# Optimization experiments

Hardware: AMD Instinct MI355X
Metric: run time of the kernel (lower is better)

## Reference

```python
import jax, jax.numpy as jnp
import numpy as np

N_EMB = 512
EMB_DIM = 64
DECAY = 0.99
EPS = 1e-5


def setup_inputs() -> dict:
    key = jax.random.key(0)
    k1, k2 = jax.random.split(key)
    x = jax.random.normal(k1, (32, EMB_DIM, 64, 64), dtype=jnp.float32)
    weight = jax.random.uniform(k2, (EMB_DIM, N_EMB), dtype=jnp.float32)  # rd_init=True: torch.rand(emb_dim, n_emb)
    cluster_size = jnp.zeros((N_EMB,), dtype=jnp.float32)
    embed_avg = weight  # buffer initialized as embed.clone()
    return {"x": x, "weight": weight, "cluster_size": cluster_size, "embed_avg": embed_avg}


def reference(x, weight, cluster_size, embed_avg):
    B, D, H, W = x.shape
    n_emb = weight.shape[1]
    # (B, D, H, W) -> (N, D) tokens
    flat = jnp.transpose(x, (0, 2, 3, 1)).reshape(-1, D)
    dist = (jnp.sum(flat * flat, axis=1, keepdims=True)
            - 2.0 * (flat @ weight)
            + jnp.sum(weight * weight, axis=0)[None, :])
    argmin = jnp.argmin(dist, axis=1)                      # (N,)
    quant = jnp.take(weight.T, argmin, axis=0)             # gather -> (N, D)
    result = jnp.transpose(quant.reshape(B, H, W, D), (0, 3, 1, 2))  # (B, D, H, W)

    # --- EMA codebook update (training branch) ---
    ones = jnp.ones(argmin.shape, dtype=x.dtype)
    n_idx = jax.ops.segment_sum(ones, argmin, num_segments=n_emb)    # onehot.sum(0)
    n_idx = jnp.where(n_idx == 0, jnp.ones_like(n_idx), n_idx)       # clamp empty clusters to 1
    new_cluster_size = DECAY * cluster_size + (1.0 - DECAY) * n_idx
    embed_sum = jax.ops.segment_sum(flat, argmin, num_segments=n_emb).T  # flatten.T @ onehot -> (D, n_emb)
    new_embed_avg = DECAY * embed_avg + (1.0 - DECAY) * embed_sum
    n = jnp.sum(new_cluster_size)
    cs = (new_cluster_size + EPS) / (n + n_emb * EPS) * n
    new_weight = new_embed_avg / cs[None, :]

    return result, argmin.reshape(B, H, W), new_weight, new_cluster_size, new_embed_avg
```

## Files before the change

kernel.cpp:

```cpp
#include <hip/hip_runtime.h>

#define NEMB 512
#define EMB 64
#define BSTR 262144
#define DECAYF 0.99f
#define OMDF 0.01f
#define EPSF 1e-5f
#define GAP_T 0.012f
#define QCAP 32768

typedef __attribute__((ext_vector_type(8))) short bf16x8;
typedef __attribute__((ext_vector_type(4))) float f32x4;

__device__ __forceinline__ unsigned short f2bf(float f) {
    unsigned u = __float_as_uint(f);
    return (unsigned short)((u + 0x7FFFu + ((u >> 16) & 1u)) >> 16);
}
__device__ __forceinline__ float bf2f(unsigned short h) {
    return __uint_as_float(((unsigned)h) << 16);
}

__global__ void prep_kernel(const float* __restrict__ w,
                            unsigned short* __restrict__ wh, unsigned short* __restrict__ wl,
                            float* __restrict__ wsq,
                            float* __restrict__ cnt_ws, float* __restrict__ es_region,
                            unsigned* __restrict__ gcnt) {
    int j = threadIdx.x;
    if (blockIdx.x < 8) {
        int d0 = blockIdx.x << 3;
        bf16x8 hb, lb;
#pragma unroll
        for (int i = 0; i < 8; ++i) {
            float v = w[(d0 + i) * NEMB + j];
            unsigned short h = f2bf(v);
            hb[i] = (short)h;
            lb[i] = (short)f2bf(v - bf2f(h));
        }
        *(bf16x8*)(wh + j * EMB + d0) = hb;
        *(bf16x8*)(wl + j * EMB + d0) = lb;
    } else {
        float s = 0.f;
#pragma unroll
        for (int d = 0; d < EMB; ++d) { float v = w[d * NEMB + j]; s = fmaf(v, v, s); }
        wsq[j] = s;
        cnt_ws[j] = 0.f;
        if (j == 0) *gcnt = 0u;
#pragma unroll
        for (int k = j; k < 32768; k += 512) es_region[k] = 0.f;
    }
}

#define UPD(S1, J1, S2, J2, s_, j_) do { \
    if (s_ < S1 || (s_ == S1 && j_ < J1)) { S2 = S1; J2 = J1; S1 = s_; J1 = j_; } \
    else if (s_ < S2 || (s_ == S2 && j_ < J2)) { S2 = s_; J2 = j_; } } while (0)

__global__ __launch_bounds__(128, 4) void vq_main(
    const float* __restrict__ x,
    const unsigned short* __restrict__ wh, const unsigned short* __restrict__ wl,
    const float* __restrict__ wsq,
    float* __restrict__ out_arg, unsigned* __restrict__ gcnt, int* __restrict__ queue)
{
    __shared__ float wsq_s[NEMB];

    const int tid = threadIdx.x;
    const int blk = blockIdx.x;
    const int b   = blk >> 6;
    const int h   = blk & 63;
    const int t0  = b * 4096 + h * 64;
    const float* xrow = x + b * BSTR + h * 64;

    wsq_s[tid]       = wsq[tid];
    wsq_s[tid + 128] = wsq[tid + 128];
    wsq_s[tid + 256] = wsq[tid + 256];
    wsq_s[tid + 384] = wsq[tid + 384];

    const int lane = tid & 63;
    const int wave = tid >> 6;
    const int l15  = lane & 15;
    const int quad = lane >> 4;
    const int wbase = wave << 5;

    bf16x8 ah[2][2], al[2][2];
    float  xq[2][4];
#pragma unroll
    for (int mt = 0; mt < 2; ++mt) {
        const float* xp = xrow + wbase + (mt << 4) + l15;
        float s = 0.f;
#pragma unroll
        for (int ks = 0; ks < 2; ++ks) {
            const int d0 = (ks << 5) + (quad << 3);
            bf16x8 hh, ll;
#pragma unroll
            for (int i = 0; i < 8; ++i) {
                float v = xp[(d0 + i) * 4096];
                s = fmaf(v, v, s);
                unsigned short hb = f2bf(v);
                hh[i] = (short)hb;
                ll[i] = (short)f2bf(v - bf2f(hb));
            }
            ah[mt][ks] = hh; al[mt][ks] = ll;
        }
        s += __shfl_xor(s, 16, 64);
        s += __shfl_xor(s, 32, 64);
#pragma unroll
        for (int r = 0; r < 4; ++r)
            xq[mt][r] = __shfl(s, (quad << 2) + r, 64);
    }
    __syncthreads();

    float v1[2][4], v2[2][4];
    int   j1[2][4];
#pragma unroll
    for (int mt = 0; mt < 2; ++mt)
#pragma unroll
        for (int r = 0; r < 4; ++r) { v1[mt][r] = 3.4e38f; v2[mt][r] = 3.4e38f; j1[mt][r] = 0; }

    const unsigned short* ph = wh + l15 * EMB + (quad << 3);
    const unsigned short* pl = wl + l15 * EMB + (quad << 3);
    bf16x8 nb0 = *(const bf16x8*)(ph);
    bf16x8 nb1 = *(const bf16x8*)(ph + 32);
    bf16x8 nb2 = *(const bf16x8*)(pl);
    bf16x8 nb3 = *(const bf16x8*)(pl + 32);

#pragma unroll 2
    for (int it = 0; it < 32; ++it) {
        bf16x8 b0 = nb0, b1 = nb1, b2 = nb2, b3 = nb3;
        if (it != 31) {
            ph += 1024; pl += 1024;
            nb0 = *(const bf16x8*)(ph);
            nb1 = *(const bf16x8*)(ph + 32);
            nb2 = *(const bf16x8*)(pl);
            nb3 = *(const bf16x8*)(pl + 32);
        }
        const int n = (it << 4) + l15;
        float wq = wsq_s[n];

        f32x4 acc0 = (f32x4){0.f, 0.f, 0.f, 0.f};
        f32x4 acc1 = (f32x4){0.f, 0.f, 0.f, 0.f};
        acc0 = __builtin_amdgcn_mfma_f32_16x16x32_bf16(ah[0][0], b0, acc0, 0, 0, 0);
        acc1 = __builtin_amdgcn_mfma_f32_16x16x32_bf16(ah[1][0], b0, acc1, 0, 0, 0);
        acc0 = __builtin_amdgcn_mfma_f32_16x16x32_bf16(ah[0][1], b1, acc0, 0, 0, 0);
        acc1 = __builtin_amdgcn_mfma_f32_16x16x32_bf16(ah[1][1], b1, acc1, 0, 0, 0);
        acc0 = __builtin_amdgcn_mfma_f32_16x16x32_bf16(ah[0][0], b2, acc0, 0, 0, 0);
        acc1 = __builtin_amdgcn_mfma_f32_16x16x32_bf16(ah[1][0], b2, acc1, 0, 0, 0);
        acc0 = __builtin_amdgcn_mfma_f32_16x16x32_bf16(ah[0][1], b3, acc0, 0, 0, 0);
        acc1 = __builtin_amdgcn_mfma_f32_16x16x32_bf16(ah[1][1], b3, acc1, 0, 0, 0);
        acc0 = __builtin_amdgcn_mfma_f32_16x16x32_bf16(al[0][0], b0, acc0, 0, 0, 0);
        acc1 = __builtin_amdgcn_mfma_f32_16x16x32_bf16(al[1][0], b0, acc1, 0, 0, 0);
        acc0 = __builtin_amdgcn_mfma_f32_16x16x32_bf16(al[0][1], b1, acc0, 0, 0, 0);
        acc1 = __builtin_amdgcn_mfma_f32_16x16x32_bf16(al[1][1], b1, acc1, 0, 0, 0);

#pragma unroll
        for (int r = 0; r < 4; ++r) {
            float s0 = fmaf(-2.f, acc0[r], xq[0][r] + wq);
            bool p0 = s0 < v1[0][r];
            float mx0 = fmaxf(s0, v1[0][r]);
            v1[0][r] = fminf(s0, v1[0][r]);
            v2[0][r] = fminf(v2[0][r], mx0);
            j1[0][r] = p0 ? n : j1[0][r];

            float s1 = fmaf(-2.f, acc1[r], xq[1][r] + wq);
            bool p1 = s1 < v1[1][r];
            float mx1 = fmaxf(s1, v1[1][r]);
            v1[1][r] = fminf(s1, v1[1][r]);
            v2[1][r] = fminf(v2[1][r], mx1);
            j1[1][r] = p1 ? n : j1[1][r];
        }
    }

#pragma unroll
    for (int mt = 0; mt < 2; ++mt)
#pragma unroll
        for (int r = 0; r < 4; ++r) {
            float a1 = v1[mt][r], a2 = v2[mt][r];
            int   aj = j1[mt][r];
#pragma unroll
            for (int msk = 1; msk < 16; msk <<= 1) {
                float o1 = __shfl_xor(a1, msk, 64);
                int   oj = __shfl_xor(aj, msk, 64);
                float o2 = __shfl_xor(a2, msk, 64);
                bool take = (o1 < a1) || (o1 == a1 && oj < aj);
                float mx = fmaxf(a1, o1);
                a2 = fminf(fminf(a2, o2), mx);
                a1 = fminf(a1, o1);
                aj = take ? oj : aj;
            }
            v1[mt][r] = a1; v2[mt][r] = a2; j1[mt][r] = aj;
        }

    if (l15 == 0) {
#pragma unroll
        for (int mt = 0; mt < 2; ++mt)
#pragma unroll
            for (int r = 0; r < 4; ++r) {
                int gt = t0 + wbase + (mt << 4) + (quad << 2) + r;
                out_arg[gt] = (float)j1[mt][r];
                if (v2[mt][r] - v1[mt][r] < GAP_T) {
                    unsigned idx = atomicAdd(gcnt, 1u);
                    if (idx < QCAP) queue[idx] = gt;
                }
            }
    }
}

__global__ __launch_bounds__(256) void refine_kernel(
    const float* __restrict__ x, const float* __restrict__ w,
    const float* __restrict__ wsq, const unsigned* __restrict__ gcnt,
    const int* __restrict__ queue, float* __restrict__ out_arg)
{
    __shared__ float wsq_s[NEMB];
    const int tid = threadIdx.x;
    wsq_s[tid] = wsq[tid];
    wsq_s[tid + 256] = wsq[tid + 256];
    __syncthreads();

    unsigned nfu = *gcnt;
    const int nf = (int)(nfu < (unsigned)QCAP ? nfu : (unsigned)QCAP);
    const int lane = tid & 63;
    const int gw = (blockIdx.x << 2) + (tid >> 6);

    for (int i = gw; i < nf; i += 1024) {
        const int t = queue[i];
        const int b = t >> 12, pos = t & 4095;
        float xd = x[b * BSTR + lane * 4096 + pos];
        float xqv = xd * xd;
#pragma unroll
        for (int mk = 1; mk < 64; mk <<= 1) xqv += __shfl_xor(xqv, mk, 64);

        float accv[8];
#pragma unroll
        for (int k = 0; k < 8; ++k) accv[k] = 0.f;
#pragma unroll 4
        for (int d = 0; d < EMB; ++d) {
            float4 wa = *(const float4*)(w + d * NEMB + (lane << 2));
            float4 wb = *(const float4*)(w + d * NEMB + 256 + (lane << 2));
            float xv = __shfl(xd, d, 64);
            accv[0] = fmaf(xv, wa.x, accv[0]);
            accv[1] = fmaf(xv, wa.y, accv[1]);
            accv[2] = fmaf(xv, wa.z, accv[2]);
            accv[3] = fmaf(xv, wa.w, accv[3]);
            accv[4] = fmaf(xv, wb.x, accv[4]);
            accv[5] = fmaf(xv, wb.y, accv[5]);
            accv[6] = fmaf(xv, wb.z, accv[6]);
            accv[7] = fmaf(xv, wb.w, accv[7]);
        }

        float S1 = 3.4e38f, S2 = 3.4e38f; int J1 = 0, J2 = 0;
#pragma unroll
        for (int k = 0; k < 8; ++k) {
            int j = (k < 4) ? ((lane << 2) + k) : (256 + (lane << 2) + k - 4);
            float s = (xqv - 2.f * accv[k]) + wsq_s[j];
            UPD(S1, J1, S2, J2, s, j);
        }
#pragma unroll
        for (int mk = 1; mk < 64; mk <<= 1) {
            float os1 = __shfl_xor(S1, mk, 64); int oj1 = __shfl_xor(J1, mk, 64);
            float os2 = __shfl_xor(S2, mk, 64); int oj2 = __shfl_xor(J2, mk, 64);
            UPD(S1, J1, S2, J2, os1, oj1);
            UPD(S1, J1, S2, J2, os2, oj2);
        }

        int jm = J1;
        if (S2 - S1 < 1e-3f) {
            float w1 = w[lane * NEMB + J1];
            float w2 = w[lane * NEMB + J2];
            double e1 = (double)w1 * (double)w1 - 2.0 * (double)xd * (double)w1;
            double e2 = (double)w2 * (double)w2 - 2.0 * (double)xd * (double)w2;
#pragma unroll
            for (int mk = 1; mk < 64; mk <<= 1) {
                e1 += __shfl_xor(e1, mk, 64);
                e2 += __shfl_xor(e2, mk, 64);
            }
            if (e2 < e1 || (e2 == e1 && J2 < J1)) jm = J2;
        }
        if (lane == 0) out_arg[t] = (float)jm;
    }
}

__global__ __launch_bounds__(256) void finish_kernel(
    const float* __restrict__ x, const float* __restrict__ w, const float* __restrict__ arg,
    float* __restrict__ out_result,
    float* __restrict__ es, float* __restrict__ cnt)
{
    __shared__ float wrow[NEMB];
    __shared__ float acc[8][513];
    const int tid = threadIdx.x;
    const int grp = blockIdx.x >> 5;
    const int chunk = blockIdx.x & 31;

    float* af = &acc[0][0];
#pragma unroll
    for (int k = tid; k < 8 * 513; k += 256) af[k] = 0.f;
    if (grp < 64) {
        wrow[tid] = w[grp * NEMB + tid];
        wrow[tid + 256] = w[grp * NEMB + tid + 256];
    }
    __syncthreads();

    const int c = tid & 7;
    const int tbase = chunk << 12;
    if (grp < 64) {
        const int d = grp;
#pragma unroll 2
        for (int it = 0; it < 4; ++it) {
            int t = tbase + (it << 10) + (tid << 2);
            int o = (t >> 12) * BSTR + d * 4096 + (t & 4095);
            float4 a4 = *(const float4*)(arg + t);
            float4 x4 = *(const float4*)(x + o);
            int j0 = (int)a4.x, j1 = (int)a4.y, j2 = (int)a4.z, j3 = (int)a4.w;
            atomicAdd(&acc[c][j0], x4.x);
            atomicAdd(&acc[c][j1], x4.y);
            atomicAdd(&acc[c][j2], x4.z);
            atomicAdd(&acc[c][j3], x4.w);
            float4 r4 = {wrow[j0], wrow[j1], wrow[j2], wrow[j3]};
            *(float4*)(out_result + o) = r4;
        }
    } else {
#pragma unroll 2
        for (int it = 0; it < 4; ++it) {
            int t = tbase + (it << 10) + (tid << 2);
            float4 a4 = *(const float4*)(arg + t);
            atomicAdd(&acc[c][(int)a4.x], 1.0f);
            atomicAdd(&acc[c][(int)a4.y], 1.0f);
            atomicAdd(&acc[c][(int)a4.z], 1.0f);
            atomicAdd(&acc[c][(int)a4.w], 1.0f);
        }
    }
    __syncthreads();

    float* dst = (grp < 64) ? (es + grp * NEMB) : cnt;
#pragma unroll
    for (int k = 0; k < 2; ++k) {
        int j = tid + (k << 8);
        float v = acc[0][j] + acc[1][j] + acc[2][j] + acc[3][j]
                + acc[4][j] + acc[5][j] + acc[6][j] + acc[7][j];
        if (v != 0.f) atomicAdd(&dst[j], v);
    }
}

__global__ void finalize_kernel(const float* __restrict__ cs_in, const float* __restrict__ avg_in,
                                const float* __restrict__ cnt_ws,
                                float* __restrict__ out_w, float* __restrict__ out_ncs,
                                float* __restrict__ avg_io ) {
    __shared__ float red[NEMB];
    const int j = threadIdx.x;
    const int d = blockIdx.x;
    float c = cnt_ws[j];
    float nidx = (c == 0.f) ? 1.f : c;
    float ncs = DECAYF * cs_in[j] + OMDF * nidx;
    red[j] = ncs;
    __syncthreads();
    for (int s = 256; s > 0; s >>= 1) {
        if (j < s) red[j] += red[j + s];
        __syncthreads();
    }
    float n = red[0];
    float csj = (ncs + EPSF) / (n + (float)NEMB * EPSF) * n;
    int o = d * NEMB + j;
    float esv = avg_io[o];
    float navg = DECAYF * avg_in[o] + OMDF * esv;
    avg_io[o] = navg;
    out_w[o] = navg / csj;
    if (d == 0) out_ncs[j] = ncs;
}

extern "C" void kernel_launch(void* const* d_in, const int* in_sizes, int n_in,
                              void* d_out, int out_size, void* d_ws, size_t ws_size,
                              hipStream_t stream) {
    (void)in_sizes; (void)n_in; (void)out_size; (void)ws_size;
    const float* x   = (const float*)d_in[0];
    const float* w   = (const float*)d_in[1];
    const float* cs  = (const float*)d_in[2];
    const float* avg = (const float*)d_in[3];

    float* out = (float*)d_out;
    float* out_result = out;
    float* out_arg    = out + 8388608;
    float* out_w      = out + 8519680;
    float* out_ncs    = out + 8552448;
    float* out_avg    = out + 8552960;

    char* wsb = (char*)d_ws;
    unsigned short* wh = (unsigned short*)wsb;
    unsigned short* wl = (unsigned short*)(wsb + 65536);
    float* wsq      = (float*)(wsb + 131072);
    float* cnt_ws   = (float*)(wsb + 133120);
    unsigned* gcnt  = (unsigned*)(wsb + 135168);
    int* queue      = (int*)(wsb + 135232);

    prep_kernel<<<9, 512, 0, stream>>>(w, wh, wl, wsq, cnt_ws, out_avg, gcnt);
    vq_main<<<2048, 128, 0, stream>>>(x, wh, wl, wsq, out_arg, gcnt, queue);
    refine_kernel<<<256, 256, 0, stream>>>(x, w, wsq, gcnt, queue, out_arg);
    finish_kernel<<<2080, 256, 0, stream>>>(x, w, out_arg, out_result, out_avg, cnt_ws);
    finalize_kernel<<<64, 512, 0, stream>>>(cs, avg, cnt_ws, out_w, out_ncs, out_avg);
}
```

Before: 214.3 us.

## Stage x and codebook tiles in LDS, enlarge vq and finish blocks

Measured after the change: 189.7 us. -11.5%, faster.

```diff
diff --git a/kernel.cpp b/kernel.cpp
--- a/kernel.cpp
+++ b/kernel.cpp
@@ -54,25 +54,42 @@
     if (s_ < S1 || (s_ == S1 && j_ < J1)) { S2 = S1; J2 = J1; S1 = s_; J1 = j_; } \
     else if (s_ < S2 || (s_ == S2 && j_ < J2)) { S2 = s_; J2 = j_; } } while (0)
 
-__global__ __launch_bounds__(128, 4) void vq_main(
+__global__ __launch_bounds__(512, 4) void vq_main(
     const float* __restrict__ x,
     const unsigned short* __restrict__ wh, const unsigned short* __restrict__ wl,
     const float* __restrict__ wsq,
     float* __restrict__ out_arg, unsigned* __restrict__ gcnt, int* __restrict__ queue)
 {
+    __shared__ __align__(16) unsigned char ubuf[65536];
     __shared__ float wsq_s[NEMB];
+    __shared__ float xsq_s[256];
+
+    float* xt = (float*)ubuf;
+    unsigned short* whs = (unsigned short*)ubuf;
+    unsigned short* wls = whs + 16384;
 
     const int tid = threadIdx.x;
     const int blk = blockIdx.x;
-    const int b   = blk >> 6;
-    const int h   = blk & 63;
-    const int t0  = b * 4096 + h * 64;
-    const float* xrow = x + b * BSTR + h * 64;
-
-    wsq_s[tid]       = wsq[tid];
-    wsq_s[tid + 128] = wsq[tid + 128];
-    wsq_s[tid + 256] = wsq[tid + 256];
-    wsq_s[tid + 384] = wsq[tid + 384];
+    const int b    = blk >> 4;
+    const int hgrp = blk & 15;
+    const int t0 = b * 4096 + hgrp * 256;
+    const float* xbase = x + b * BSTR + hgrp * 256;
+
+#pragma unroll
+    for (int it = 0; it < 8; ++it) {
+        int idx = tid + (it << 9);
+        int d = idx >> 6, q = idx & 63;
+        *(float4*)(xt + d * 256 + (q << 2)) = *(const float4*)(xbase + d * 4096 + (q << 2));
+    }
+    wsq_s[tid] = wsq[tid];
+    __syncthreads();
+
+    if (tid < 256) {
+        float s = 0.f;
+#pragma unroll
+        for (int d = 0; d < EMB; ++d) { float v = xt[d * 256 + tid]; s = fmaf(v, v, s); }
+        xsq_s[tid] = s;
+    }
 
     const int lane = tid & 63;
     const int wave = tid >> 6;
@@ -81,32 +98,31 @@
     const int wbase = wave << 5;
 
     bf16x8 ah[2][2], al[2][2];
-    float  xq[2][4];
 #pragma unroll
     for (int mt = 0; mt < 2; ++mt) {
-        const float* xp = xrow + wbase + (mt << 4) + l15;
-        float s = 0.f;
+        int m = wbase + (mt << 4) + l15;
 #pragma unroll
         for (int ks = 0; ks < 2; ++ks) {
-            const int d0 = (ks << 5) + (quad << 3);
+            int k0 = (ks << 5) + (quad << 3);
             bf16x8 hh, ll;
 #pragma unroll
             for (int i = 0; i < 8; ++i) {
-                float v = xp[(d0 + i) * 4096];
-                s = fmaf(v, v, s);
-                unsigned short hb = f2bf(v);
-                hh[i] = (short)hb;
-                ll[i] = (short)f2bf(v - bf2f(hb));
+                float v = xt[(k0 + i) * 256 + m];
+                unsigned short h = f2bf(v);
+                hh[i] = (short)h;
+                ll[i] = (short)f2bf(v - bf2f(h));
             }
             ah[mt][ks] = hh; al[mt][ks] = ll;
         }
-        s += __shfl_xor(s, 16, 64);
-        s += __shfl_xor(s, 32, 64);
+    }
+    __syncthreads();
+
+    float xq[2][4];
+#pragma unroll
+    for (int mt = 0; mt < 2; ++mt)
 #pragma unroll
         for (int r = 0; r < 4; ++r)
-            xq[mt][r] = __shfl(s, (quad << 2) + r, 64);
-    }
-    __syncthreads();
+            xq[mt][r] = xsq_s[wbase + (mt << 4) + (quad << 2) + r];
 
     float v1[2][4], v2[2][4];
     int   j1[2][4];
@@ -115,57 +131,70 @@
 #pragma unroll
         for (int r = 0; r < 4; ++r) { v1[mt][r] = 3.4e38f; v2[mt][r] = 3.4e38f; j1[mt][r] = 0; }
 
-    const unsigned short* ph = wh + l15 * EMB + (quad << 3);
-    const unsigned short* pl = wl + l15 * EMB + (quad << 3);
-    bf16x8 nb0 = *(const bf16x8*)(ph);
-    bf16x8 nb1 = *(const bf16x8*)(ph + 32);
-    bf16x8 nb2 = *(const bf16x8*)(pl);
-    bf16x8 nb3 = *(const bf16x8*)(pl + 32);
-
+    const int m7 = l15 & 7;
+    const int s0off = ((quad ^ m7) << 3);
+    const int s1off = (((4 | quad) ^ m7) << 3);
+
+    for (int half = 0; half < 2; ++half) {
+#pragma unroll
+        for (int it = 0; it < 8; ++it) {
+            int e = tid + (it << 9);
+            int arr  = e >> 11;
+            int win  = e & 2047;
+            int row  = win >> 3;
+            int slot = win & 7;
+            const unsigned short* src =
+                (arr ? wl : wh) + ((half << 8) + row) * EMB + (slot << 3);
+            bf16x8 v = *(const bf16x8*)src;
+            unsigned short* dstb = arr ? wls : whs;
+            *(bf16x8*)(dstb + row * EMB + ((slot ^ (row & 7)) << 3)) = v;
+        }
+        __syncthreads();
+
+        const int nbase = half << 8;
 #pragma unroll 2
-    for (int it = 0; it < 32; ++it) {
-        bf16x8 b0 = nb0, b1 = nb1, b2 = nb2, b3 = nb3;
-        if (it != 31) {
-            ph += 1024; pl += 1024;
-            nb0 = *(const bf16x8*)(ph);
-            nb1 = *(const bf16x8*)(ph + 32);
-            nb2 = *(const bf16x8*)(pl);
-            nb3 = *(const bf16x8*)(pl + 32);
-        }
-        const int n = (it << 4) + l15;
-        float wq = wsq_s[n];
-
-        f32x4 acc0 = (f32x4){0.f, 0.f, 0.f, 0.f};
-        f32x4 acc1 = (f32x4){0.f, 0.f, 0.f, 0.f};
-        acc0 = __builtin_amdgcn_mfma_f32_16x16x32_bf16(ah[0][0], b0, acc0, 0, 0, 0);
-        acc1 = __builtin_amdgcn_mfma_f32_16x16x32_bf16(ah[1][0], b0, acc1, 0, 0, 0);
-        acc0 = __builtin_amdgcn_mfma_f32_16x16x32_bf16(ah[0][1], b1, acc0, 0, 0, 0);
-        acc1 = __builtin_amdgcn_mfma_f32_16x16x32_bf16(ah[1][1], b1, acc1, 0, 0, 0);
-        acc0 = __builtin_amdgcn_mfma_f32_16x16x32_bf16(ah[0][0], b2, acc0, 0, 0, 0);
-        acc1 = __builtin_amdgcn_mfma_f32_16x16x32_bf16(ah[1][0], b2, acc1, 0, 0, 0);
-        acc0 = __builtin_amdgcn_mfma_f32_16x16x32_bf16(ah[0][1], b3, acc0, 0, 0, 0);
-        acc1 = __builtin_amdgcn_mfma_f32_16x16x32_bf16(ah[1][1], b3, acc1, 0, 0, 0);
-        acc0 = __builtin_amdgcn_mfma_f32_16x16x32_bf16(al[0][0], b0, acc0, 0, 0, 0);
-        acc1 = __builtin_amdgcn_mfma_f32_16x16x32_bf16(al[1][0], b0, acc1, 0, 0, 0);
-        acc0 = __builtin_amdgcn_mfma_f32_16x16x32_bf16(al[0][1], b1, acc0, 0, 0, 0);
-        acc1 = __builtin_amdgcn_mfma_f32_16x16x32_bf16(al[1][1], b1, acc1, 0, 0, 0);
-
-#pragma unroll
-        for (int r = 0; r < 4; ++r) {
-            float s0 = fmaf(-2.f, acc0[r], xq[0][r] + wq);
-            bool p0 = s0 < v1[0][r];
-            float mx0 = fmaxf(s0, v1[0][r]);
-            v1[0][r] = fminf(s0, v1[0][r]);
-            v2[0][r] = fminf(v2[0][r], mx0);
-            j1[0][r] = p0 ? n : j1[0][r];
-
-            float s1 = fmaf(-2.f, acc1[r], xq[1][r] + wq);
-            bool p1 = s1 < v1[1][r];
-            float mx1 = fmaxf(s1, v1[1][r]);
-            v1[1][r] = fminf(s1, v1[1][r]);
-            v2[1][r] = fminf(v2[1][r], mx1);
-            j1[1][r] = p1 ? n : j1[1][r];
-        }
+        for (int it = 0; it < 16; ++it) {
+            const int ib = ((it << 4) + l15) << 6;
+            bf16x8 b0 = *(const bf16x8*)(whs + ib + s0off);
+            bf16x8 b1 = *(const bf16x8*)(whs + ib + s1off);
+            bf16x8 b2 = *(const bf16x8*)(wls + ib + s0off);
+            bf16x8 b3 = *(const bf16x8*)(wls + ib + s1off);
+            const int n = nbase + (it << 4) + l15;
+            float wq = wsq_s[n];
+
+            f32x4 acc0 = (f32x4){0.f, 0.f, 0.f, 0.f};
+            f32x4 acc1 = (f32x4){0.f, 0.f, 0.f, 0.f};
+            acc0 = __builtin_amdgcn_mfma_f32_16x16x32_bf16(ah[0][0], b0, acc0, 0, 0, 0);
+            acc1 = __builtin_amdgcn_mfma_f32_16x16x32_bf16(ah[1][0], b0, acc1, 0, 0, 0);
+            acc0 = __builtin_amdgcn_mfma_f32_16x16x32_bf16(ah[0][1], b1, acc0, 0, 0, 0);
+            acc1 = __builtin_amdgcn_mfma_f32_16x16x32_bf16(ah[1][1], b1, acc1, 0, 0, 0);
+            acc0 = __builtin_amdgcn_mfma_f32_16x16x32_bf16(ah[0][0], b2, acc0, 0, 0, 0);
+            acc1 = __builtin_amdgcn_mfma_f32_16x16x32_bf16(ah[1][0], b2, acc1, 0, 0, 0);
+            acc0 = __builtin_amdgcn_mfma_f32_16x16x32_bf16(ah[0][1], b3, acc0, 0, 0, 0);
+            acc1 = __builtin_amdgcn_mfma_f32_16x16x32_bf16(ah[1][1], b3, acc1, 0, 0, 0);
+            acc0 = __builtin_amdgcn_mfma_f32_16x16x32_bf16(al[0][0], b0, acc0, 0, 0, 0);
+            acc1 = __builtin_amdgcn_mfma_f32_16x16x32_bf16(al[1][0], b0, acc1, 0, 0, 0);
+            acc0 = __builtin_amdgcn_mfma_f32_16x16x32_bf16(al[0][1], b1, acc0, 0, 0, 0);
+            acc1 = __builtin_amdgcn_mfma_f32_16x16x32_bf16(al[1][1], b1, acc1, 0, 0, 0);
+
+#pragma unroll
+            for (int r = 0; r < 4; ++r) {
+                float s0 = fmaf(-2.f, acc0[r], xq[0][r] + wq);
+                bool p0 = s0 < v1[0][r];
+                float mx0 = fmaxf(s0, v1[0][r]);
+                v1[0][r] = fminf(s0, v1[0][r]);
+                v2[0][r] = fminf(v2[0][r], mx0);
+                j1[0][r] = p0 ? n : j1[0][r];
+
+                float s1 = fmaf(-2.f, acc1[r], xq[1][r] + wq);
+                bool p1 = s1 < v1[1][r];
+                float mx1 = fmaxf(s1, v1[1][r]);
+                v1[1][r] = fminf(s1, v1[1][r]);
+                v2[1][r] = fminf(v2[1][r], mx1);
+                j1[1][r] = p1 ? n : j1[1][r];
+            }
+        }
+        __syncthreads();
     }
 
 #pragma unroll
@@ -277,64 +306,62 @@
     }
 }
 
-__global__ __launch_bounds__(256) void finish_kernel(
+__global__ __launch_bounds__(512) void finish_kernel(
     const float* __restrict__ x, const float* __restrict__ w, const float* __restrict__ arg,
     float* __restrict__ out_result,
     float* __restrict__ es, float* __restrict__ cnt)
 {
-    __shared__ float wrow[NEMB];
-    __shared__ float acc[8][513];
+    __shared__ float wrow8[8 * 512];
+    __shared__ float acc8[8 * 513];
+    __shared__ float cacc[513];
     const int tid = threadIdx.x;
-    const int grp = blockIdx.x >> 5;
-    const int chunk = blockIdx.x & 31;
-
-    float* af = &acc[0][0];
-#pragma unroll
-    for (int k = tid; k < 8 * 513; k += 256) af[k] = 0.f;
-    if (grp < 64) {
-        wrow[tid] = w[grp * NEMB + tid];
-        wrow[tid + 256] = w[grp * NEMB + tid + 256];
-    }
-    __syncthreads();
-
-    const int c = tid & 7;
-    const int tbase = chunk << 12;
-    if (grp < 64) {
-        const int d = grp;
-#pragma unroll 2
-        for (int it = 0; it < 4; ++it) {
-            int t = tbase + (it << 10) + (tid << 2);
-            int o = (t >> 12) * BSTR + d * 4096 + (t & 4095);
-            float4 a4 = *(const float4*)(arg + t);
-            float4 x4 = *(const float4*)(x + o);
-            int j0 = (int)a4.x, j1 = (int)a4.y, j2 = (int)a4.z, j3 = (int)a4.w;
-            atomicAdd(&acc[c][j0], x4.x);
-            atomicAdd(&acc[c][j1], x4.y);
-            atomicAdd(&acc[c][j2], x4.z);
-            atomicAdd(&acc[c][j3], x4.w);
-            float4 r4 = {wrow[j0], wrow[j1], wrow[j2], wrow[j3]};
-            *(float4*)(out_result + o) = r4;
-        }
-    } else {
-#pragma unroll 2
-        for (int it = 0; it < 4; ++it) {
-            int t = tbase + (it << 10) + (tid << 2);
-            float4 a4 = *(const float4*)(arg + t);
-            atomicAdd(&acc[c][(int)a4.x], 1.0f);
-            atomicAdd(&acc[c][(int)a4.y], 1.0f);
-            atomicAdd(&acc[c][(int)a4.z], 1.0f);
-            atomicAdd(&acc[c][(int)a4.w], 1.0f);
-        }
-    }
-    __syncthreads();
-
-    float* dst = (grp < 64) ? (es + grp * NEMB) : cnt;
-#pragma unroll
-    for (int k = 0; k < 2; ++k) {
-        int j = tid + (k << 8);
-        float v = acc[0][j] + acc[1][j] + acc[2][j] + acc[3][j]
-                + acc[4][j] + acc[5][j] + acc[6][j] + acc[7][j];
-        if (v != 0.f) atomicAdd(&dst[j], v);
+    const int grp = blockIdx.x >> 6;
+    const int chunk = blockIdx.x & 63;
+
+#pragma unroll
+    for (int d = 0; d < 8; ++d) {
+        wrow8[(d << 9) + tid] = w[((grp << 3) + d) * NEMB + tid];
+        acc8[d * 513 + tid] = 0.f;
+    }
+    if (tid < 8) acc8[tid * 513 + 512] = 0.f;
+    cacc[tid] = 0.f;
+    if (tid == 0) cacc[512] = 0.f;
+    __syncthreads();
+
+    const int t = (chunk << 11) + (tid << 2);
+    const int b = t >> 12;
+    const int o = b * BSTR + (t & 4095);
+    float4 a4 = *(const float4*)(arg + t);
+    int j0 = (int)a4.x, j1 = (int)a4.y, j2 = (int)a4.z, j3 = (int)a4.w;
+    if (grp == 0) {
+        atomicAdd(&cacc[j0], 1.f);
+        atomicAdd(&cacc[j1], 1.f);
+        atomicAdd(&cacc[j2], 1.f);
+        atomicAdd(&cacc[j3], 1.f);
+    }
+#pragma unroll
+    for (int d = 0; d < 8; ++d) {
+        const int dg = (grp << 3) + d;
+        float4 x4 = *(const float4*)(x + o + dg * 4096);
+        float* ad = acc8 + d * 513;
+        atomicAdd(&ad[j0], x4.x);
+        atomicAdd(&ad[j1], x4.y);
+        atomicAdd(&ad[j2], x4.z);
+        atomicAdd(&ad[j3], x4.w);
+        float4 r4 = {wrow8[(d << 9) + j0], wrow8[(d << 9) + j1],
+                     wrow8[(d << 9) + j2], wrow8[(d << 9) + j3]};
+        *(float4*)(out_result + o + dg * 4096) = r4;
+    }
+    __syncthreads();
+
+#pragma unroll
+    for (int d = 0; d < 8; ++d) {
+        float v = acc8[d * 513 + tid];
+        if (v != 0.f) atomicAdd(&es[((grp << 3) + d) * NEMB + tid], v);
+    }
+    if (grp == 0) {
+        float cv = cacc[tid];
+        if (cv != 0.f) atomicAdd(&cnt[tid], cv);
     }
 }
 
@@ -389,8 +416,8 @@
     int* queue      = (int*)(wsb + 135232);
 
     prep_kernel<<<9, 512, 0, stream>>>(w, wh, wl, wsq, cnt_ws, out_avg, gcnt);
-    vq_main<<<2048, 128, 0, stream>>>(x, wh, wl, wsq, out_arg, gcnt, queue);
+    vq_main<<<512, 512, 0, stream>>>(x, wh, wl, wsq, out_arg, gcnt, queue);
     refine_kernel<<<256, 256, 0, stream>>>(x, w, wsq, gcnt, queue, out_arg);
-    finish_kernel<<<2080, 256, 0, stream>>>(x, w, out_arg, out_result, out_avg, cnt_ws);
+    finish_kernel<<<512, 512, 0, stream>>>(x, w, out_arg, out_result, out_avg, cnt_ws);
     finalize_kernel<<<64, 512, 0, stream>>>(cs, avg, cnt_ws, out_w, out_ncs, out_avg);
 }
```
